# Optimization experiments

Hardware: AMD Instinct MI355X
Metric: run time of the kernel (lower is better)

## Reference

```python
import jax, jax.numpy as jnp
import numpy as np

BN_EPS = 1e-5
NORM_EPS = 1e-12  # F.normalize eps


def setup_inputs() -> dict:
    key = jax.random.key(0)
    ks = jax.random.split(key, 4)
    B, C1, H, W = 32, 2048, 32, 32
    D1, D2, NC = 1024, 256, 1000
    x = jax.random.normal(ks[0], (B, C1, H, W), dtype=jnp.float32)
    w1 = jax.random.normal(ks[1], (D1, C1), dtype=jnp.float32) * 0.01  # init_weights normal 0.01
    gamma = jnp.ones((D1,), dtype=jnp.float32)
    beta = jnp.zeros((D1,), dtype=jnp.float32)
    w2 = jax.random.normal(ks[2], (D2, D1), dtype=jnp.float32) * 0.01
    prototypes = jax.random.normal(ks[3], (NC, D2), dtype=jnp.float32)
    return {"x": x, "w1": w1, "gamma": gamma, "beta": beta, "w2": w2, "prototypes": prototypes}


def _l2_normalize(v, axis):
    n = jnp.sqrt(jnp.sum(v * v, axis=axis, keepdims=True))
    return v / jnp.maximum(n, NORM_EPS)


def reference(x, w1, gamma, beta, w2, prototypes):
    # 1x1 conv (no bias) == channel matmul
    h = jnp.einsum('bchw,dc->bdhw', x, w1)  # [B,D1,H,W]
    # BatchNorm2d (training-mode batch stats, affine)
    mean = jnp.mean(h, axis=(0, 2, 3), keepdims=True)
    var = jnp.var(h, axis=(0, 2, 3), keepdims=True)
    h = (h - mean) * jax.lax.rsqrt(var + BN_EPS)
    h = h * gamma[None, :, None, None] + beta[None, :, None, None]
    h = jax.nn.relu(h)
    # final 1x1 conv
    f = jnp.einsum('bchw,dc->bdhw', h, w2)  # [B,D2,H,W]
    B, D, H, W = f.shape
    f = f.reshape(B, D, H * W)  # flatten(2)
    # L2-normalize over channel dim per spatial position, and prototypes per row
    f_norm = _l2_normalize(f, axis=1)           # [B,D,HW]
    p_norm = _l2_normalize(prototypes, axis=1)  # [N,D]
    # einsum('bdc,nd->bnc').sum(-1) == contract d then sum c in one fused einsum
    sim = jnp.einsum('bdc,nd->bn', f_norm, p_norm)  # [B,N]
    return sim
```

## Files before the change

kernel.cpp:

```cpp
#include <hip/hip_runtime.h>

typedef __bf16 bf16;
typedef __bf16 bf16x4 __attribute__((ext_vector_type(4)));
typedef __bf16 bf16x8 __attribute__((ext_vector_type(8)));
typedef float  f32x4  __attribute__((ext_vector_type(4)));

__device__ inline void async_copy16(void* lds, const void* g) {
  __builtin_amdgcn_global_load_lds((const __attribute__((address_space(1))) void*)g,
                                   (__attribute__((address_space(3))) void*)lds,
                                   16, 0, 0);
}

__global__ __launch_bounds__(256)
void f2bf_kernel(const float* __restrict__ in, bf16* __restrict__ out, int n4) {
  int i = blockIdx.x * 256 + threadIdx.x;
  if (i < n4) {
    float4 v = ((const float4*)in)[i];
    bf16x4 o;
    o[0] = (bf16)v.x; o[1] = (bf16)v.y; o[2] = (bf16)v.z; o[3] = (bf16)v.w;
    ((bf16x4*)out)[i] = o;
  }
}

__global__ __launch_bounds__(256)
void transpose_convert(const float* __restrict__ x, bf16* __restrict__ xb) {
  __shared__ float tile[64][65];
  const int tx = threadIdx.x & 15;
  const int ty = threadIdx.x >> 4;
  const int b   = blockIdx.z;
  const int c0  = blockIdx.y * 64;
  const int hw0 = blockIdx.x * 64;
  const float* xp = x + ((size_t)b * 2048 + c0) * 1024 + hw0;
#pragma unroll
  for (int i = 0; i < 4; ++i) {
    const int c = i * 16 + ty;
    const float4 v = *(const float4*)(xp + (size_t)c * 1024 + tx * 4);
    tile[c][tx * 4 + 0] = v.x; tile[c][tx * 4 + 1] = v.y;
    tile[c][tx * 4 + 2] = v.z; tile[c][tx * 4 + 3] = v.w;
  }
  __syncthreads();
  bf16* op = xb + ((size_t)b * 1024 + hw0) * 2048 + c0;
#pragma unroll
  for (int i = 0; i < 4; ++i) {
    const int hw = i * 16 + ty;
    bf16x4 o;
    o[0] = (bf16)tile[tx * 4 + 0][hw];
    o[1] = (bf16)tile[tx * 4 + 1][hw];
    o[2] = (bf16)tile[tx * 4 + 2][hw];
    o[3] = (bf16)tile[tx * 4 + 3][hw];
    *(bf16x4*)(op + (size_t)hw * 2048 + tx * 4) = o;
  }
}

__global__ __launch_bounds__(256, 4)
void gemm1(const bf16* __restrict__ A, const bf16* __restrict__ Bt,
           bf16* __restrict__ Cb, float* __restrict__ S1, float* __restrict__ S2) {
  __shared__ __align__(16) bf16 As[128 * 64];
  __shared__ __align__(16) bf16 Bs[128 * 64];
  const int K = 2048, N = 1024;
  const int tid  = threadIdx.x;
  const int wave = tid >> 6;
  const int lane = tid & 63;
  const int id = blockIdx.x;
  const int bm = (id & 7) * 32 + ((id >> 3) >> 3);
  const int bn = (id >> 3) & 7;
  const int wr = wave >> 1, wc = wave & 1;
  const int srow = lane >> 3;
  const int scol = (lane & 7) ^ srow;

  f32x4 acc[4][4];
#pragma unroll
  for (int r = 0; r < 4; ++r)
#pragma unroll
    for (int c = 0; c < 4; ++c) acc[r][c] = (f32x4){0.f, 0.f, 0.f, 0.f};

  const bf16* Ag = A + (size_t)(bm * 128) * K;
  const bf16* Bg = Bt + (size_t)(bn * 128) * K;

  const int mrow = lane & 15;
  const int kq = lane >> 4;
  const int sw = mrow & 7;
  const bf16* Asw = As + (wr * 64) * 64;
  const bf16* Bsw = Bs + (wc * 64) * 64;

  for (int k0 = 0; k0 < K; k0 += 64) {
#pragma unroll
    for (int j = 0; j < 4; ++j) {
      const int row = j * 32 + wave * 8;
      async_copy16((void*)(As + row * 64),
                   (const void*)(Ag + (size_t)(row + srow) * K + k0 + scol * 8));
      async_copy16((void*)(Bs + row * 64),
                   (const void*)(Bg + (size_t)(row + srow) * K + k0 + scol * 8));
    }
    __syncthreads();
#pragma unroll
    for (int kk = 0; kk < 2; ++kk) {
      bf16x8 af[4], bfr[4];
      const int lc = kk * 4 + kq;
#pragma unroll
      for (int r = 0; r < 4; ++r)
        af[r] = *(const bf16x8*)(Asw + (r * 16 + mrow) * 64 + ((lc ^ sw) * 8));
#pragma unroll
      for (int c = 0; c < 4; ++c)
        bfr[c] = *(const bf16x8*)(Bsw + (c * 16 + mrow) * 64 + ((lc ^ sw) * 8));
#pragma unroll
      for (int r = 0; r < 4; ++r)
#pragma unroll
        for (int c = 0; c < 4; ++c)
          acc[r][c] = __builtin_amdgcn_mfma_f32_16x16x32_bf16(af[r], bfr[c], acc[r][c], 0, 0, 0);
    }
    __syncthreads();
  }

  const int crow = (lane >> 4) * 4;
  const int ccol = lane & 15;
#pragma unroll
  for (int r = 0; r < 4; ++r)
#pragma unroll
    for (int c = 0; c < 4; ++c)
#pragma unroll
      for (int i = 0; i < 4; ++i) {
        const int gm = bm * 128 + wr * 64 + r * 16 + crow + i;
        const int gn = bn * 128 + wc * 64 + c * 16 + ccol;
        Cb[(size_t)gm * N + gn] = (bf16)acc[r][c][i];
      }

  float s1[4], s2[4];
#pragma unroll
  for (int c = 0; c < 4; ++c) {
    float a = 0.f, b = 0.f;
#pragma unroll
    for (int r = 0; r < 4; ++r)
#pragma unroll
      for (int i = 0; i < 4; ++i) { const float v = acc[r][c][i]; a += v; b += v * v; }
#pragma unroll
    for (int msk = 16; msk < 64; msk <<= 1) { a += __shfl_xor(a, msk, 64); b += __shfl_xor(b, msk, 64); }
    s1[c] = a; s2[c] = b;
  }
  float* S1s = (float*)As;
  float* S2s = S1s + 256;
  if ((lane & 15) == lane) {
#pragma unroll
    for (int c = 0; c < 4; ++c) {
      S1s[wr * 128 + wc * 64 + c * 16 + lane] = s1[c];
      S2s[wr * 128 + wc * 64 + c * 16 + lane] = s2[c];
    }
  }
  __syncthreads();
  if (tid < 128) {
    atomicAdd(&S1[bn * 128 + tid], S1s[tid] + S1s[128 + tid]);
    atomicAdd(&S2[bn * 128 + tid], S2s[tid] + S2s[128 + tid]);
  }
}

__global__ __launch_bounds__(256)
void bn_finalize(const float* __restrict__ S1, const float* __restrict__ S2,
                 const float* __restrict__ gamma, const float* __restrict__ beta,
                 float* __restrict__ scale, float* __restrict__ shift) {
  const int d = blockIdx.x * 256 + threadIdx.x;
  const float inv_n = 1.0f / 32768.0f;
  const float mean = S1[d] * inv_n;
  const float var  = S2[d] * inv_n - mean * mean;
  const float rstd = rsqrtf(var + 1e-5f);
  const float sc = gamma[d] * rstd;
  scale[d] = sc;
  shift[d] = beta[d] - mean * sc;
}

__global__ __launch_bounds__(512, 4)
void gemm2f(const bf16* __restrict__ A, const bf16* __restrict__ Bt,
            const float* __restrict__ scale, const float* __restrict__ shift,
            float* __restrict__ g) {
  __shared__ __align__(16) bf16 As[128 * 64];
  __shared__ __align__(16) bf16 Bs[256 * 64];
  const int K = 1024;
  const int tid  = threadIdx.x;
  const int wave = tid >> 6;
  const int lane = tid & 63;
  const int bm = blockIdx.x;
  const int wr = wave >> 2, wc = wave & 3;
  const int srow = lane >> 3;
  const int scol = (lane & 7) ^ srow;

  f32x4 acc[4][4];
#pragma unroll
  for (int r = 0; r < 4; ++r)
#pragma unroll
    for (int c = 0; c < 4; ++c) acc[r][c] = (f32x4){0.f, 0.f, 0.f, 0.f};

  const bf16* Ag = A + (size_t)(bm * 128) * K;

  const int mrow = lane & 15;
  const int kq = lane >> 4;
  const int sw = mrow & 7;
  const bf16* Asw = As + (wr * 64) * 64;
  const bf16* Bsw = Bs + (wc * 64) * 64;

  for (int k0 = 0; k0 < K; k0 += 64) {
#pragma unroll
    for (int j = 0; j < 2; ++j) {
      const int row = wave * 16 + j * 8;
      async_copy16((void*)(As + row * 64),
                   (const void*)(Ag + (size_t)(row + srow) * K + k0 + scol * 8));
    }
#pragma unroll
    for (int j = 0; j < 4; ++j) {
      const int row = wave * 32 + j * 8;
      async_copy16((void*)(Bs + row * 64),
                   (const void*)(Bt + (size_t)(row + srow) * K + k0 + scol * 8));
    }
    __syncthreads();
#pragma unroll
    for (int kk = 0; kk < 2; ++kk) {
      const int lc = kk * 4 + kq;
      const int kbase = k0 + lc * 8;
      const float4 sc0 = *(const float4*)(scale + kbase);
      const float4 sc1 = *(const float4*)(scale + kbase + 4);
      const float4 sh0 = *(const float4*)(shift + kbase);
      const float4 sh1 = *(const float4*)(shift + kbase + 4);
      const float scv[8] = {sc0.x, sc0.y, sc0.z, sc0.w, sc1.x, sc1.y, sc1.z, sc1.w};
      const float shv[8] = {sh0.x, sh0.y, sh0.z, sh0.w, sh1.x, sh1.y, sh1.z, sh1.w};
      bf16x8 af[4], bfr[4];
#pragma unroll
      for (int r = 0; r < 4; ++r) {
        bf16x8 a = *(const bf16x8*)(Asw + (r * 16 + mrow) * 64 + ((lc ^ sw) * 8));
#pragma unroll
        for (int j = 0; j < 8; ++j)
          a[j] = (bf16)fmaxf(0.f, fmaf((float)a[j], scv[j], shv[j]));
        af[r] = a;
      }
#pragma unroll
      for (int c = 0; c < 4; ++c)
        bfr[c] = *(const bf16x8*)(Bsw + (c * 16 + mrow) * 64 + ((lc ^ sw) * 8));
#pragma unroll
      for (int r = 0; r < 4; ++r)
#pragma unroll
        for (int c = 0; c < 4; ++c)
          acc[r][c] = __builtin_amdgcn_mfma_f32_16x16x32_bf16(af[r], bfr[c], acc[r][c], 0, 0, 0);
    }
    __syncthreads();
  }

  float* ss4   = (float*)As;
  float* inv_s = ss4 + 512;
  const int q = lane >> 4;
#pragma unroll
  for (int r = 0; r < 4; ++r) {
    float ssv[4];
#pragma unroll
    for (int i = 0; i < 4; ++i) {
      float s = 0.f;
#pragma unroll
      for (int c = 0; c < 4; ++c) { const float v = acc[r][c][i]; s += v * v; }
#pragma unroll
      for (int msk = 1; msk < 16; msk <<= 1) s += __shfl_xor(s, msk, 64);
      ssv[i] = s;
    }
    if ((lane & 15) == 0)
#pragma unroll
      for (int i = 0; i < 4; ++i)
        ss4[wc * 128 + wr * 64 + r * 16 + q * 4 + i] = ssv[i];
  }
  __syncthreads();
  if (tid < 128) {
    const float rs = ss4[tid] + ss4[128 + tid] + ss4[256 + tid] + ss4[384 + tid];
    inv_s[tid] = 1.0f / fmaxf(sqrtf(rs), 1e-12f);
  }
  __syncthreads();
  const int b = bm >> 3;
  const int ccol = lane & 15;
#pragma unroll
  for (int c = 0; c < 4; ++c) {
    float gl = 0.f;
#pragma unroll
    for (int r = 0; r < 4; ++r)
#pragma unroll
      for (int i = 0; i < 4; ++i)
        gl += acc[r][c][i] * inv_s[wr * 64 + r * 16 + q * 4 + i];
#pragma unroll
    for (int msk = 16; msk < 64; msk <<= 1) gl += __shfl_xor(gl, msk, 64);
    if ((lane & 48) == 0)
      atomicAdd(&g[b * 256 + wc * 64 + c * 16 + ccol], gl);
  }
}

__global__ __launch_bounds__(256)
void sim_kernel(const float* __restrict__ g, const float* __restrict__ protos,
                float* __restrict__ out) {
  const int wave = threadIdx.x >> 6, lane = threadIdx.x & 63;
  const int n = blockIdx.x * 4 + wave;
  const float4 p = *(const float4*)(protos + (size_t)n * 256 + lane * 4);
  float ss = p.x * p.x + p.y * p.y + p.z * p.z + p.w * p.w;
#pragma unroll
  for (int msk = 1; msk < 64; msk <<= 1) ss += __shfl_xor(ss, msk, 64);
  const float inv = 1.0f / fmaxf(sqrtf(ss), 1e-12f);
  const float px = p.x * inv, py = p.y * inv, pz = p.z * inv, pw = p.w * inv;
  for (int b = 0; b < 32; ++b) {
    const float4 gv = *(const float4*)(g + b * 256 + lane * 4);
    float d = px * gv.x + py * gv.y + pz * gv.z + pw * gv.w;
#pragma unroll
    for (int msk = 1; msk < 64; msk <<= 1) d += __shfl_xor(d, msk, 64);
    if (lane == 0) out[b * 1000 + n] = d;
  }
}

extern "C" void kernel_launch(void* const* d_in, const int* in_sizes, int n_in,
                              void* d_out, int out_size, void* d_ws, size_t ws_size,
                              hipStream_t stream) {
  const float* x      = (const float*)d_in[0];
  const float* w1     = (const float*)d_in[1];
  const float* gamma  = (const float*)d_in[2];
  const float* beta   = (const float*)d_in[3];
  const float* w2     = (const float*)d_in[4];
  const float* protos = (const float*)d_in[5];
  float* out = (float*)d_out;

  char* ws = (char*)d_ws;
  bf16*  xb    = (bf16*)(ws);
  bf16*  hb    = (bf16*)(ws + (size_t)134217728);
  bf16*  w1b   = (bf16*)(ws + (size_t)201326592);
  bf16*  w2b   = (bf16*)(ws + (size_t)205520896);
  float* S1    = (float*)(ws + (size_t)206045184);
  float* S2    = (float*)(ws + (size_t)206049280);
  float* g     = (float*)(ws + (size_t)206053376);
  float* scale = (float*)(ws + (size_t)206086144);
  float* shift = (float*)(ws + (size_t)206090240);

  hipMemsetAsync(S1, 0, 40960, stream);

  f2bf_kernel<<<2048, 256, 0, stream>>>(w1, w1b, 524288);
  f2bf_kernel<<<256, 256, 0, stream>>>(w2, w2b, 65536);
  transpose_convert<<<dim3(16, 32, 32), 256, 0, stream>>>(x, xb);
  gemm1<<<2048, 256, 0, stream>>>(xb, w1b, hb, S1, S2);
  bn_finalize<<<4, 256, 0, stream>>>(S1, S2, gamma, beta, scale, shift);
  gemm2f<<<256, 512, 0, stream>>>(hb, w2b, scale, shift, g);
  sim_kernel<<<250, 256, 0, stream>>>(g, protos, out);
}
```

Baseline: 612.6 us.

## Restructure gemm1 into 256x256 tiles with 4-stage async LDS pipeline

```diff
diff --git a/kernel.cpp b/kernel.cpp
--- a/kernel.cpp
+++ b/kernel.cpp
@@ -52,104 +52,128 @@
   }
 }
 
-__global__ __launch_bounds__(256, 4)
+__global__ __launch_bounds__(512, 2)
 void gemm1(const bf16* __restrict__ A, const bf16* __restrict__ Bt,
            bf16* __restrict__ Cb, float* __restrict__ S1, float* __restrict__ S2) {
-  __shared__ __align__(16) bf16 As[128 * 64];
-  __shared__ __align__(16) bf16 Bs[128 * 64];
-  const int K = 2048, N = 1024;
+  __shared__ __align__(16) bf16 As[4 * 8192];
+  __shared__ __align__(16) bf16 Bs[4 * 8192];
+  const int K = 2048, N = 1024, NT = 64;
   const int tid  = threadIdx.x;
   const int wave = tid >> 6;
   const int lane = tid & 63;
   const int id = blockIdx.x;
-  const int bm = (id & 7) * 32 + ((id >> 3) >> 3);
-  const int bn = (id >> 3) & 7;
-  const int wr = wave >> 1, wc = wave & 1;
-  const int srow = lane >> 3;
-  const int scol = (lane & 7) ^ srow;
-
-  f32x4 acc[4][4];
-#pragma unroll
-  for (int r = 0; r < 4; ++r)
+  const int bn = (id >> 3) & 3;
+  const int bm = (id & 7) * 16 + (id >> 5);
+  const int wr = wave >> 2, wc = wave & 3;
+
+  const int srl = lane >> 3;
+  const int sc  = (lane & 7) ^ srl;
+  const int sgr = 2 * (wave * 8 + srl) + (sc >> 2);
+  const int sk  = (sc & 3) * 8;
+  const bf16* Ag = A  + (size_t)(bm * 256 + sgr) * K + sk;
+  const bf16* Bg = Bt + (size_t)(bn * 256 + sgr) * K + sk;
+  const int ldst = wave * 1024 + lane * 16;
+
+  const int mrow = lane & 15;
+  const int kq   = lane >> 4;
+  const int srA  = mrow >> 1;
+  const int pch  = (((mrow & 1) << 2) + kq) ^ srA;
+  const int aoff = (wr * 64 + srA) * 128 + pch * 16;
+  const int boff = (wc * 32 + srA) * 128 + pch * 16;
+
+  f32x4 acc[8][4];
+#pragma unroll
+  for (int r = 0; r < 8; ++r)
 #pragma unroll
     for (int c = 0; c < 4; ++c) acc[r][c] = (f32x4){0.f, 0.f, 0.f, 0.f};
 
-  const bf16* Ag = A + (size_t)(bm * 128) * K;
-  const bf16* Bg = Bt + (size_t)(bn * 128) * K;
-
-  const int mrow = lane & 15;
-  const int kq = lane >> 4;
-  const int sw = mrow & 7;
-  const bf16* Asw = As + (wr * 64) * 64;
-  const bf16* Bsw = Bs + (wc * 64) * 64;
-
-  for (int k0 = 0; k0 < K; k0 += 64) {
-#pragma unroll
-    for (int j = 0; j < 4; ++j) {
-      const int row = j * 32 + wave * 8;
-      async_copy16((void*)(As + row * 64),
-                   (const void*)(Ag + (size_t)(row + srow) * K + k0 + scol * 8));
-      async_copy16((void*)(Bs + row * 64),
-                   (const void*)(Bg + (size_t)(row + srow) * K + k0 + scol * 8));
-    }
-    __syncthreads();
-#pragma unroll
-    for (int kk = 0; kk < 2; ++kk) {
-      bf16x8 af[4], bfr[4];
-      const int lc = kk * 4 + kq;
-#pragma unroll
-      for (int r = 0; r < 4; ++r)
-        af[r] = *(const bf16x8*)(Asw + (r * 16 + mrow) * 64 + ((lc ^ sw) * 8));
-#pragma unroll
-      for (int c = 0; c < 4; ++c)
-        bfr[c] = *(const bf16x8*)(Bsw + (c * 16 + mrow) * 64 + ((lc ^ sw) * 8));
-#pragma unroll
-      for (int r = 0; r < 4; ++r)
-#pragma unroll
-        for (int c = 0; c < 4; ++c)
-          acc[r][c] = __builtin_amdgcn_mfma_f32_16x16x32_bf16(af[r], bfr[c], acc[r][c], 0, 0, 0);
-    }
-    __syncthreads();
-  }
-
-  const int crow = (lane >> 4) * 4;
-  const int ccol = lane & 15;
-#pragma unroll
-  for (int r = 0; r < 4; ++r)
+#define STAGE(tt) do {                                                        \
+    const int s_ = (tt) & 3;                                                  \
+    const bf16* a_ = Ag + (tt) * 32;                                          \
+    const bf16* b_ = Bg + (tt) * 32;                                          \
+    char* da_ = (char*)As + s_ * 16384 + ldst;                                \
+    char* db_ = (char*)Bs + s_ * 16384 + ldst;                                \
+    async_copy16(da_,        a_);                                             \
+    async_copy16(da_ + 8192, a_ + (size_t)128 * K);                           \
+    async_copy16(db_,        b_);                                             \
+    async_copy16(db_ + 8192, b_ + (size_t)128 * K);                           \
+  } while (0)
+
+#define COMPUTE(tt) do {                                                      \
+    const char* Ab_ = (const char*)As + ((tt) & 3) * 16384 + aoff;            \
+    const char* Bb_ = (const char*)Bs + ((tt) & 3) * 16384 + boff;            \
+    bf16x8 af[8], bfr[4];                                                     \
+    _Pragma("unroll")                                                         \
+    for (int c = 0; c < 4; ++c) bfr[c] = *(const bf16x8*)(Bb_ + c * 1024);    \
+    _Pragma("unroll")                                                         \
+    for (int r = 0; r < 8; ++r) af[r] = *(const bf16x8*)(Ab_ + r * 1024);     \
+    __builtin_amdgcn_s_setprio(1);                                            \
+    _Pragma("unroll")                                                         \
+    for (int r = 0; r < 8; ++r)                                               \
+      _Pragma("unroll")                                                       \
+      for (int c = 0; c < 4; ++c)                                             \
+        acc[r][c] = __builtin_amdgcn_mfma_f32_16x16x32_bf16(af[r], bfr[c],    \
+                                                            acc[r][c], 0, 0, 0); \
+    __builtin_amdgcn_s_setprio(0);                                            \
+  } while (0)
+
+  STAGE(0); STAGE(1); STAGE(2);
+  asm volatile("s_waitcnt vmcnt(8)" ::: "memory");
+  __builtin_amdgcn_s_barrier();
+  __builtin_amdgcn_sched_barrier(0);
+
+  for (int t = 0; t < NT - 3; ++t) {
+    STAGE(t + 3);
+    COMPUTE(t);
+    asm volatile("s_waitcnt vmcnt(8)" ::: "memory");
+    __builtin_amdgcn_s_barrier();
+    __builtin_amdgcn_sched_barrier(0);
+  }
+  COMPUTE(NT - 3);
+  asm volatile("s_waitcnt vmcnt(4)" ::: "memory");
+  __builtin_amdgcn_s_barrier();
+  __builtin_amdgcn_sched_barrier(0);
+  COMPUTE(NT - 2);
+  asm volatile("s_waitcnt vmcnt(0)" ::: "memory");
+  __builtin_amdgcn_s_barrier();
+  __builtin_amdgcn_sched_barrier(0);
+  COMPUTE(NT - 1);
+  __builtin_amdgcn_s_barrier();
+
+#undef STAGE
+#undef COMPUTE
+
+#pragma unroll
+  for (int r = 0; r < 8; ++r)
 #pragma unroll
     for (int c = 0; c < 4; ++c)
 #pragma unroll
       for (int i = 0; i < 4; ++i) {
-        const int gm = bm * 128 + wr * 64 + r * 16 + crow + i;
-        const int gn = bn * 128 + wc * 64 + c * 16 + ccol;
+        const int gm = bm * 256 + wr * 128 + r * 16 + kq * 4 + i;
+        const int gn = bn * 256 + wc * 64 + c * 16 + mrow;
         Cb[(size_t)gm * N + gn] = (bf16)acc[r][c][i];
       }
 
-  float s1[4], s2[4];
+  float* S1s = (float*)As;
+  float* S2s = S1s + 512;
 #pragma unroll
   for (int c = 0; c < 4; ++c) {
     float a = 0.f, b = 0.f;
 #pragma unroll
-    for (int r = 0; r < 4; ++r)
+    for (int r = 0; r < 8; ++r)
 #pragma unroll
       for (int i = 0; i < 4; ++i) { const float v = acc[r][c][i]; a += v; b += v * v; }
 #pragma unroll
     for (int msk = 16; msk < 64; msk <<= 1) { a += __shfl_xor(a, msk, 64); b += __shfl_xor(b, msk, 64); }
-    s1[c] = a; s2[c] = b;
-  }
-  float* S1s = (float*)As;
-  float* S2s = S1s + 256;
-  if ((lane & 15) == lane) {
-#pragma unroll
-    for (int c = 0; c < 4; ++c) {
-      S1s[wr * 128 + wc * 64 + c * 16 + lane] = s1[c];
-      S2s[wr * 128 + wc * 64 + c * 16 + lane] = s2[c];
+    if (lane < 16) {
+      S1s[wr * 256 + wc * 64 + c * 16 + lane] = a;
+      S2s[wr * 256 + wc * 64 + c * 16 + lane] = b;
     }
   }
   __syncthreads();
-  if (tid < 128) {
-    atomicAdd(&S1[bn * 128 + tid], S1s[tid] + S1s[128 + tid]);
-    atomicAdd(&S2[bn * 128 + tid], S2s[tid] + S2s[128 + tid]);
+  if (tid < 256) {
+    atomicAdd(&S1[bn * 256 + tid], S1s[tid] + S1s[256 + tid]);
+    atomicAdd(&S2[bn * 256 + tid], S2s[tid] + S2s[256 + tid]);
   }
 }
 
@@ -331,7 +355,7 @@
   f2bf_kernel<<<2048, 256, 0, stream>>>(w1, w1b, 524288);
   f2bf_kernel<<<256, 256, 0, stream>>>(w2, w2b, 65536);
   transpose_convert<<<dim3(16, 32, 32), 256, 0, stream>>>(x, xb);
-  gemm1<<<2048, 256, 0, stream>>>(xb, w1b, hb, S1, S2);
+  gemm1<<<512, 512, 0, stream>>>(xb, w1b, hb, S1, S2);
   bn_finalize<<<4, 256, 0, stream>>>(S1, S2, gamma, beta, scale, shift);
   gemm2f<<<256, 512, 0, stream>>>(hb, w2b, scale, shift, g);
   sim_kernel<<<250, 256, 0, stream>>>(g, protos, out);
```

New measurement: 648.7 us. 5.9% more time.

## Restructure gemm1 into 256x128 tiles with triple-buffered async LDS pipeline

Applied to the files above, without the earlier changes.

```diff
diff --git a/kernel.cpp b/kernel.cpp
--- a/kernel.cpp
+++ b/kernel.cpp
@@ -52,21 +52,33 @@
   }
 }
 
-__global__ __launch_bounds__(256, 4)
+__global__ __launch_bounds__(512, 2)
 void gemm1(const bf16* __restrict__ A, const bf16* __restrict__ Bt,
            bf16* __restrict__ Cb, float* __restrict__ S1, float* __restrict__ S2) {
-  __shared__ __align__(16) bf16 As[128 * 64];
-  __shared__ __align__(16) bf16 Bs[128 * 64];
-  const int K = 2048, N = 1024;
+  __shared__ __align__(16) bf16 As[3 * 16384];
+  __shared__ __align__(16) bf16 Bs[3 * 8192];
+  const int K = 2048, N = 1024, NT = 32;
   const int tid  = threadIdx.x;
   const int wave = tid >> 6;
   const int lane = tid & 63;
   const int id = blockIdx.x;
-  const int bm = (id & 7) * 32 + ((id >> 3) >> 3);
-  const int bn = (id >> 3) & 7;
+  const int q  = id >> 3;
+  const int bn = q & 7;
+  const int bm = (id & 7) * 16 + (q >> 3);
   const int wr = wave >> 1, wc = wave & 1;
-  const int srow = lane >> 3;
-  const int scol = (lane & 7) ^ srow;
+
+  const int srl = lane >> 3;
+  const int sch = (lane & 7) ^ srl;
+  const int srow = wave * 8 + srl;
+  const bf16* Ag = A  + (size_t)(bm * 256 + srow) * K + sch * 8;
+  const bf16* Bg = Bt + (size_t)(bn * 128 + srow) * K + sch * 8;
+  const int ldst = wave * 1024 + lane * 16;
+
+  const int mrow = lane & 15;
+  const int kq   = lane >> 4;
+  const int sw   = mrow & 7;
+  const int aoff = (wr * 64 + mrow) * 128;
+  const int boff = (wc * 64 + mrow) * 128;
 
   f32x4 acc[4][4];
 #pragma unroll
@@ -74,58 +86,100 @@
 #pragma unroll
     for (int c = 0; c < 4; ++c) acc[r][c] = (f32x4){0.f, 0.f, 0.f, 0.f};
 
-  const bf16* Ag = A + (size_t)(bm * 128) * K;
-  const bf16* Bg = Bt + (size_t)(bn * 128) * K;
-
-  const int mrow = lane & 15;
-  const int kq = lane >> 4;
-  const int sw = mrow & 7;
-  const bf16* Asw = As + (wr * 64) * 64;
-  const bf16* Bsw = Bs + (wc * 64) * 64;
-
-  for (int k0 = 0; k0 < K; k0 += 64) {
-#pragma unroll
-    for (int j = 0; j < 4; ++j) {
-      const int row = j * 32 + wave * 8;
-      async_copy16((void*)(As + row * 64),
-                   (const void*)(Ag + (size_t)(row + srow) * K + k0 + scol * 8));
-      async_copy16((void*)(Bs + row * 64),
-                   (const void*)(Bg + (size_t)(row + srow) * K + k0 + scol * 8));
-    }
-    __syncthreads();
-#pragma unroll
-    for (int kk = 0; kk < 2; ++kk) {
-      bf16x8 af[4], bfr[4];
-      const int lc = kk * 4 + kq;
-#pragma unroll
-      for (int r = 0; r < 4; ++r)
-        af[r] = *(const bf16x8*)(Asw + (r * 16 + mrow) * 64 + ((lc ^ sw) * 8));
+#define STA3(slot, tt) do {                                                   \
+    char* da_ = (char*)As + (slot) * 32768 + ldst;                            \
+    const bf16* a_ = Ag + (size_t)(tt) * 64;                                  \
+    async_copy16(da_,         a_);                                            \
+    async_copy16(da_ + 8192,  a_ + (size_t)64 * K);                           \
+    async_copy16(da_ + 16384, a_ + (size_t)128 * K);                          \
+  } while (0)
+#define STB3(slot, tt) do {                                                   \
+    char* da_ = (char*)As + (slot) * 32768 + ldst;                            \
+    char* db_ = (char*)Bs + (slot) * 16384 + ldst;                            \
+    const bf16* a_ = Ag + (size_t)(tt) * 64;                                  \
+    const bf16* b_ = Bg + (size_t)(tt) * 64;                                  \
+    async_copy16(da_ + 24576, a_ + (size_t)192 * K);                          \
+    async_copy16(db_,         b_);                                            \
+    async_copy16(db_ + 8192,  b_ + (size_t)64 * K);                           \
+  } while (0)
+
+  STA3(0, 0); STB3(0, 0);
+  STA3(1, 1); STB3(1, 1);
+  asm volatile("s_waitcnt vmcnt(6)" ::: "memory");
+  __builtin_amdgcn_s_barrier();
+
+  int srd = 0;
+  int sst = 2;
+  for (int t = 0; t < NT; ++t) {
+    const char* Ab = (const char*)As + srd * 32768 + aoff;
+    const char* Bb = (const char*)Bs + srd * 16384 + boff;
+    const bool st = (t + 2 < NT);
+    bf16x8 bfr[4][2], af[2][2];
+#pragma unroll
+    for (int c = 0; c < 4; ++c)
+#pragma unroll
+      for (int kk = 0; kk < 2; ++kk)
+        bfr[c][kk] = *(const bf16x8*)(Bb + c * 2048 + ((kk * 4 + kq) ^ sw) * 16);
+#pragma unroll
+    for (int r = 0; r < 2; ++r)
+#pragma unroll
+      for (int kk = 0; kk < 2; ++kk)
+        af[r][kk] = *(const bf16x8*)(Ab + r * 2048 + ((kk * 4 + kq) ^ sw) * 16);
+    if (st) STA3(sst, t + 2);
+    __builtin_amdgcn_s_barrier();
+    asm volatile("s_waitcnt lgkmcnt(0)" ::: "memory");
+    __builtin_amdgcn_sched_barrier(0);
+    __builtin_amdgcn_s_setprio(1);
+#pragma unroll
+    for (int r = 0; r < 2; ++r)
 #pragma unroll
       for (int c = 0; c < 4; ++c)
-        bfr[c] = *(const bf16x8*)(Bsw + (c * 16 + mrow) * 64 + ((lc ^ sw) * 8));
-#pragma unroll
-      for (int r = 0; r < 4; ++r)
-#pragma unroll
-        for (int c = 0; c < 4; ++c)
-          acc[r][c] = __builtin_amdgcn_mfma_f32_16x16x32_bf16(af[r], bfr[c], acc[r][c], 0, 0, 0);
-    }
-    __syncthreads();
-  }
-
-  const int crow = (lane >> 4) * 4;
-  const int ccol = lane & 15;
+#pragma unroll
+        for (int kk = 0; kk < 2; ++kk)
+          acc[r][c] = __builtin_amdgcn_mfma_f32_16x16x32_bf16(af[r][kk], bfr[c][kk], acc[r][c], 0, 0, 0);
+    __builtin_amdgcn_s_setprio(0);
+    __builtin_amdgcn_s_barrier();
+    bf16x8 af2[2][2];
+#pragma unroll
+    for (int r = 0; r < 2; ++r)
+#pragma unroll
+      for (int kk = 0; kk < 2; ++kk)
+        af2[r][kk] = *(const bf16x8*)(Ab + (r + 2) * 2048 + ((kk * 4 + kq) ^ sw) * 16);
+    if (st) STB3(sst, t + 2);
+    __builtin_amdgcn_s_barrier();
+    asm volatile("s_waitcnt lgkmcnt(0)" ::: "memory");
+    __builtin_amdgcn_sched_barrier(0);
+    __builtin_amdgcn_s_setprio(1);
+#pragma unroll
+    for (int r = 0; r < 2; ++r)
+#pragma unroll
+      for (int c = 0; c < 4; ++c)
+#pragma unroll
+        for (int kk = 0; kk < 2; ++kk)
+          acc[r + 2][c] = __builtin_amdgcn_mfma_f32_16x16x32_bf16(af2[r][kk], bfr[c][kk], acc[r + 2][c], 0, 0, 0);
+    __builtin_amdgcn_s_setprio(0);
+    if (st) { asm volatile("s_waitcnt vmcnt(6)" ::: "memory"); }
+    else if (t + 1 < NT) { asm volatile("s_waitcnt vmcnt(0)" ::: "memory"); }
+    __builtin_amdgcn_s_barrier();
+    srd = (srd == 2) ? 0 : srd + 1;
+    sst = (sst == 2) ? 0 : sst + 1;
+  }
+#undef STA3
+#undef STB3
+
 #pragma unroll
   for (int r = 0; r < 4; ++r)
 #pragma unroll
     for (int c = 0; c < 4; ++c)
 #pragma unroll
       for (int i = 0; i < 4; ++i) {
-        const int gm = bm * 128 + wr * 64 + r * 16 + crow + i;
-        const int gn = bn * 128 + wc * 64 + c * 16 + ccol;
+        const int gm = bm * 256 + wr * 64 + r * 16 + kq * 4 + i;
+        const int gn = bn * 128 + wc * 64 + c * 16 + mrow;
         Cb[(size_t)gm * N + gn] = (bf16)acc[r][c][i];
       }
 
-  float s1[4], s2[4];
+  float* S1s = (float*)As;
+  float* S2s = S1s + 512;
 #pragma unroll
   for (int c = 0; c < 4; ++c) {
     float a = 0.f, b = 0.f;
@@ -135,21 +189,17 @@
       for (int i = 0; i < 4; ++i) { const float v = acc[r][c][i]; a += v; b += v * v; }
 #pragma unroll
     for (int msk = 16; msk < 64; msk <<= 1) { a += __shfl_xor(a, msk, 64); b += __shfl_xor(b, msk, 64); }
-    s1[c] = a; s2[c] = b;
-  }
-  float* S1s = (float*)As;
-  float* S2s = S1s + 256;
-  if ((lane & 15) == lane) {
-#pragma unroll
-    for (int c = 0; c < 4; ++c) {
-      S1s[wr * 128 + wc * 64 + c * 16 + lane] = s1[c];
-      S2s[wr * 128 + wc * 64 + c * 16 + lane] = s2[c];
+    if (lane < 16) {
+      S1s[wr * 128 + wc * 64 + c * 16 + lane] = a;
+      S2s[wr * 128 + wc * 64 + c * 16 + lane] = b;
     }
   }
   __syncthreads();
   if (tid < 128) {
-    atomicAdd(&S1[bn * 128 + tid], S1s[tid] + S1s[128 + tid]);
-    atomicAdd(&S2[bn * 128 + tid], S2s[tid] + S2s[128 + tid]);
+    const float a = S1s[tid] + S1s[128 + tid] + S1s[256 + tid] + S1s[384 + tid];
+    const float b = S2s[tid] + S2s[128 + tid] + S2s[256 + tid] + S2s[384 + tid];
+    atomicAdd(&S1[bn * 128 + tid], a);
+    atomicAdd(&S2[bn * 128 + tid], b);
   }
 }
 
@@ -331,7 +381,7 @@
   f2bf_kernel<<<2048, 256, 0, stream>>>(w1, w1b, 524288);
   f2bf_kernel<<<256, 256, 0, stream>>>(w2, w2b, 65536);
   transpose_convert<<<dim3(16, 32, 32), 256, 0, stream>>>(x, xb);
-  gemm1<<<2048, 256, 0, stream>>>(xb, w1b, hb, S1, S2);
+  gemm1<<<1024, 512, 0, stream>>>(xb, w1b, hb, S1, S2);
   bn_finalize<<<4, 256, 0, stream>>>(S1, S2, gamma, beta, scale, shift);
   gemm2f<<<256, 512, 0, stream>>>(hb, w2b, scale, shift, g);
   sim_kernel<<<250, 256, 0, stream>>>(g, protos, out);
```

After: 644.2 us. +5.2%, slower.
